# Performance work log

Measured on AMD Instinct MI355X. Metric: run time of the kernel, lower is better.

Reference implementation:

```python
import jax, jax.numpy as jnp
import numpy as np

N, E, G = 50000, 800000, 64   # nodes, edges, graphs
IN, HID, H = 128, 64, 4       # in_channels, hidden_channels, heads


def setup_inputs() -> dict:
    key = jax.random.key(0)
    ks = jax.random.split(key, 32)
    r = lambda i, shape, sc=0.05: jax.random.normal(ks[i], shape, jnp.float32) * sc
    inp = {
        "x": jax.random.normal(ks[0], (N, IN), jnp.float32),
        "edge_index": jax.random.randint(ks[1], (2, E), 0, N),
        "batch": jnp.sort(jax.random.randint(ks[2], (N,), 0, G)),
        # GATConv 1: in -> hidden, heads=4, concat
        "W1": r(3, (IN, H * HID)), "a_src1": r(4, (H, HID)), "a_dst1": r(5, (H, HID)), "b1": r(6, (H * HID,)),
        "bn1_g": 1.0 + r(7, (H * HID,)), "bn1_b": r(8, (H * HID,)), "bn1_m": r(9, (H * HID,)),
        "bn1_v": jax.random.uniform(ks[10], (H * HID,), jnp.float32, 0.5, 1.5),
        # GATConv 2: hidden*heads -> hidden, heads=4, concat
        "W2": r(11, (H * HID, H * HID)), "a_src2": r(12, (H, HID)), "a_dst2": r(13, (H, HID)), "b2": r(14, (H * HID,)),
        "bn2_g": 1.0 + r(15, (H * HID,)), "bn2_b": r(16, (H * HID,)), "bn2_m": r(17, (H * HID,)),
        "bn2_v": jax.random.uniform(ks[18], (H * HID,), jnp.float32, 0.5, 1.5),
        # GATConv 3: hidden*heads -> hidden, heads=1
        "W3": r(19, (H * HID, HID)), "a_src3": r(20, (1, HID)), "a_dst3": r(21, (1, HID)), "b3": r(22, (HID,)),
        # projection MLP: Linear(2*hidden, hidden) -> ReLU -> Linear(hidden, hidden)
        "P1": r(23, (2 * HID, HID)), "pb1": r(24, (HID,)),
        "P2": r(25, (HID, HID)), "pb2": r(26, (HID,)),
    }
    return inp


def _gat_conv(x, src, dst, n, W, a_s, a_d, b, concat):
    """PyG-style GATConv (eval mode). src/dst already include self-loops."""
    Hh, C = a_s.shape
    h = (x @ W).reshape(n, Hh, C)                       # [N, H, C]
    al_s = jnp.einsum('nhc,hc->nh', h, a_s)             # [N, H]
    al_d = jnp.einsum('nhc,hc->nh', h, a_d)             # [N, H]
    e = jax.nn.leaky_relu(al_s[src] + al_d[dst], 0.2)   # [E', H]
    # segment softmax over incoming edges of each dst node
    m = jax.ops.segment_max(e, dst, num_segments=n)     # [N, H] (finite: self-loops)
    ex = jnp.exp(e - m[dst])
    den = jax.ops.segment_sum(ex, dst, num_segments=n)
    alpha = ex / den[dst]                               # [E', H]
    out = jax.ops.segment_sum(h[src] * alpha[..., None], dst, num_segments=n)  # [N, H, C]
    out = out.reshape(n, Hh * C) if concat else out.mean(axis=1)
    return out + b


def _bn(x, g, b, m, v):
    return (x - m) * jax.lax.rsqrt(v + 1e-5) * g + b


def _forward(x, edge_index, batch,
             W1, a_src1, a_dst1, b1, bn1_g, bn1_b, bn1_m, bn1_v,
             W2, a_src2, a_dst2, b2, bn2_g, bn2_b, bn2_m, bn2_v,
             W3, a_src3, a_dst3, b3, P1, pb1, P2, pb2):
    n = x.shape[0]
    loop = jnp.arange(n)
    src = jnp.concatenate([edge_index[0], loop])        # add_self_loops=True
    dst = jnp.concatenate([edge_index[1], loop])
    h = _gat_conv(x, src, dst, n, W1, a_src1, a_dst1, b1, True)
    h = jax.nn.elu(_bn(h, bn1_g, bn1_b, bn1_m, bn1_v))  # dropout inactive in eval
    h = _gat_conv(h, src, dst, n, W2, a_src2, a_dst2, b2, True)
    h = jax.nn.elu(_bn(h, bn2_g, bn2_b, bn2_m, bn2_v))
    h = _gat_conv(h, src, dst, n, W3, a_src3, a_dst3, b3, False)  # heads=1
    x_max = jax.ops.segment_max(h, batch, num_segments=G)
    cnt = jax.ops.segment_sum(jnp.ones((n, 1), h.dtype), batch, num_segments=G)
    x_mean = jax.ops.segment_sum(h, batch, num_segments=G) / jnp.maximum(cnt, 1.0)
    z = jnp.concatenate([x_max, x_mean], axis=1)        # [G, 2*HID]
    z = jax.nn.relu(z @ P1 + pb1)
    return z @ P2 + pb2                                  # [G, HID]


def reference(x, edge_index, batch,
              W1, a_src1, a_dst1, b1, bn1_g, bn1_b, bn1_m, bn1_v,
              W2, a_src2, a_dst2, b2, bn2_g, bn2_b, bn2_m, bn2_v,
              W3, a_src3, a_dst3, b3, P1, pb1, P2, pb2):
    return _forward(x, edge_index, batch,
                    W1, a_src1, a_dst1, b1, bn1_g, bn1_b, bn1_m, bn1_v,
                    W2, a_src2, a_dst2, b2, bn2_g, bn2_b, bn2_m, bn2_v,
                    W3, a_src3, a_dst3, b3, P1, pb1, P2, pb2)
```

## Files before the change

### kernel.cpp

```cpp
#include <hip/hip_runtime.h>

typedef unsigned int uint;
typedef unsigned short ushort;

#define NFIX 50000
#define EFIX 800000
#define GFIX 64
#define BCAP 64
#define DCAP 128
#define WSTRIDE 136
#define PSL 16

__device__ __forceinline__ float bflo(uint u) { return __uint_as_float(u << 16); }
__device__ __forceinline__ float bfhi(uint u) { return __uint_as_float(u & 0xffff0000u); }
__device__ __forceinline__ float bf1(ushort u) { return __uint_as_float(((uint)u) << 16); }
__device__ __forceinline__ ushort f2bf(float f) {
    uint u = __float_as_uint(f);
    u += 0x7fffu + ((u >> 16) & 1u);
    return (ushort)(u >> 16);
}
__device__ __forceinline__ float lrelu(float x) { return fmaxf(x, 0.2f * x); }

typedef __attribute__((ext_vector_type(8))) short bf16x8;
typedef __attribute__((ext_vector_type(4))) float f32x4;
union U16B { uint4 u; bf16x8 v; };

__global__ void detect_idx_width(const int* __restrict__ ei, int* __restrict__ flag) {
    const int lane = threadIdx.x & 63;
    int v = (lane < 16) ? ei[2 * lane + 1] : 0;
    unsigned long long any = __ballot(v != 0);
    if (lane == 0 && blockIdx.x == 0) *flag = (any == 0ULL) ? 1 : 0;
}

__device__ __forceinline__ int ld_idx(const int* __restrict__ p, long i, int w64) {
    return w64 ? p[2 * i] : p[i];
}

__device__ __forceinline__ int frag_off(int k, int c, int K) {
    return ((c >> 4) * (K >> 5) + (k >> 5)) * 512 + ((c & 15) + 16 * ((k >> 3) & 3)) * 8 + (k & 7);
}

#define WJ1 (128 * 256)
#define WJ2 (256 * 256)
#define WJ3 (256 * 64)
#define BPJOBS (EFIX + WJ1 + WJ2 + WJ3)
__global__ void build_prep(const int* __restrict__ ei, const int* __restrict__ flag,
                           int* __restrict__ cnt, ushort* __restrict__ ssb,
                           const float* __restrict__ W1, ushort* __restrict__ Wf1,
                           const float* __restrict__ W2, ushort* __restrict__ Wf2,
                           const float* __restrict__ W3, ushort* __restrict__ Wf3) {
    int i = blockIdx.x * 256 + threadIdx.x;
    if (i < EFIX) {
        const int w64 = *flag;
        int d = ld_idx(ei, (long)EFIX + i, w64);
        int s = ld_idx(ei, i, w64);
        int slot = atomicAdd(&cnt[d], 1);
        if (slot < BCAP) ssb[d * BCAP + slot] = (ushort)s;
    } else {
        int j = i - EFIX;
        if (j < WJ1) {
            int k = j >> 8, c = j & 255;
            Wf1[frag_off(k, c, 128)] = f2bf(W1[j]);
        } else if ((j -= WJ1) < WJ2) {
            int k = j >> 8, c = j & 255;
            Wf2[frag_off(k, c, 256)] = f2bf(W2[j]);
        } else if ((j -= WJ2) < WJ3) {
            int k = j >> 6, c = j & 63;
            Wf3[frag_off(k, c, 256)] = f2bf(W3[j]);
        }
    }
}

template <int K, int NI, int HAL, bool F32A>
__global__ __launch_bounds__(256) void gemm_frag(const void* __restrict__ Xv,
                                                 const ushort* __restrict__ Wf,
                                                 const float* __restrict__ as_,
                                                 const float* __restrict__ ad_,
                                                 ushort* __restrict__ Hout,
                                                 float* __restrict__ als,
                                                 float* __restrict__ ald, int M) {
    constexpr int NC = NI * 16 * 4;
    constexpr int LOG2K = (K == 256) ? 8 : 7;
    __shared__ ushort sa[64][K + 8];
    __shared__ float s_ps[4][64];
    __shared__ float s_pd[4][64];

    const int tid = threadIdx.x;
    const int wave = tid >> 6;
    const int lane = tid & 63;
    const int rowBase = blockIdx.x * 64;
    const int colBase = wave * (NI * 16);
    const int tr = lane & 15;
    const int kq = (lane >> 4) * 8;

    if constexpr (F32A) {
        const float* srcf = (const float*)Xv;
#pragma unroll
        for (int it = 0; it < (64 * K) / 1024; ++it) {
            int linear = it * 1024 + tid * 4;
            int row = rowBase + (linear >> LOG2K);
            int col = linear & (K - 1);
            row = row < M ? row : M - 1;
            float4 v = *(const float4*)(srcf + (size_t)row * K + col);
            ushort4 o; o.x = f2bf(v.x); o.y = f2bf(v.y); o.z = f2bf(v.z); o.w = f2bf(v.w);
            *(ushort4*)(&sa[linear >> LOG2K][col]) = o;
        }
    } else {
        const ushort* src = (const ushort*)Xv + (size_t)rowBase * K;
#pragma unroll
        for (int it = 0; it < (64 * K) / 2048; ++it) {
            int linear = it * 2048 + tid * 8;
            int row = linear >> LOG2K;
            int col = linear & (K - 1);
            *(uint4*)(&sa[row][col]) = *(const uint4*)(src + linear);
        }
    }
    __syncthreads();

    f32x4 acc[4][NI];
#pragma unroll
    for (int i = 0; i < 4; ++i)
#pragma unroll
        for (int j = 0; j < NI; ++j) acc[i][j] = (f32x4){0.f, 0.f, 0.f, 0.f};

    const ushort* bp[NI];
#pragma unroll
    for (int ni = 0; ni < NI; ++ni)
        bp[ni] = Wf + ((size_t)(colBase / 16 + ni) * (K / 32)) * 512 + lane * 8;

    for (int k0 = 0; k0 < K; k0 += 32) {
        bf16x8 a[4], b[NI];
#pragma unroll
        for (int mi = 0; mi < 4; ++mi) { U16B t; t.u = *(const uint4*)(&sa[mi * 16 + tr][k0 + kq]); a[mi] = t.v; }
#pragma unroll
        for (int ni = 0; ni < NI; ++ni) { U16B t; t.u = *(const uint4*)(bp[ni] + (k0 >> 5) * 512); b[ni] = t.v; }
#pragma unroll
        for (int mi = 0; mi < 4; ++mi)
#pragma unroll
            for (int ni = 0; ni < NI; ++ni)
                acc[mi][ni] = __builtin_amdgcn_mfma_f32_16x16x32_bf16(a[mi], b[ni], acc[mi][ni], 0, 0, 0);
    }

    const int orow = (lane >> 4) * 4;
    const int ocol = colBase + tr;
#pragma unroll
    for (int mi = 0; mi < 4; ++mi) {
#pragma unroll
        for (int r = 0; r < 4; ++r) {
            int row = rowBase + mi * 16 + orow + r;
            if (row < M) {
#pragma unroll
                for (int ni = 0; ni < NI; ++ni)
                    Hout[(size_t)row * NC + ocol + ni * 16] = f2bf(acc[mi][ni][r]);
            }
        }
    }

    float asv[NI], adv[NI];
#pragma unroll
    for (int ni = 0; ni < NI; ++ni) {
        asv[ni] = as_[colBase + ni * 16 + tr];
        adv[ni] = ad_[colBase + ni * 16 + tr];
    }
#pragma unroll
    for (int mi = 0; mi < 4; ++mi) {
#pragma unroll
        for (int r = 0; r < 4; ++r) {
            float ps = 0.f, pd = 0.f;
#pragma unroll
            for (int ni = 0; ni < NI; ++ni) {
                ps += acc[mi][ni][r] * asv[ni];
                pd += acc[mi][ni][r] * adv[ni];
            }
#pragma unroll
            for (int off = 1; off < 16; off <<= 1) {
                ps += __shfl_xor(ps, off, 64);
                pd += __shfl_xor(pd, off, 64);
            }
            if constexpr (HAL == 4) {
                int row = rowBase + mi * 16 + orow + r;
                if (tr == 0 && row < M) {
                    als[(size_t)row * 4 + wave] = ps;
                    ald[(size_t)row * 4 + wave] = pd;
                }
            } else {
                if (tr == 0) {
                    s_ps[wave][mi * 16 + orow + r] = ps;
                    s_pd[wave][mi * 16 + orow + r] = pd;
                }
            }
        }
    }
    if constexpr (HAL == 1) {
        __syncthreads();
        if (tid < 64) {
            int row = rowBase + tid;
            if (row < M) {
                als[row] = s_ps[0][tid] + s_ps[1][tid] + s_ps[2][tid] + s_ps[3][tid];
                ald[row] = s_pd[0][tid] + s_pd[1][tid] + s_pd[2][tid] + s_pd[3][tid];
            }
        }
    }
}

template <int H_, int C>
__global__ __launch_bounds__(256) void gat_gather(
    const ushort* __restrict__ hb, const float* __restrict__ als, const float* __restrict__ ald,
    const int* __restrict__ cnt, const ushort* __restrict__ ssb,
    const float* __restrict__ bias, const float* __restrict__ bng, const float* __restrict__ bnb,
    const float* __restrict__ bnm, const float* __restrict__ bnv,
    ushort* __restrict__ xnext, int n) {
    constexpr int TC = H_ * C;
    constexpr int CPL = TC / 64;
    constexpr int GW = 64 / H_;
    constexpr int KMAX = DCAP / GW;
    constexpr int SHIFT = 8;
    __shared__ float s_w[4][H_ * WSTRIDE];
    __shared__ int s_idx[4][DCAP];
    const int wv = threadIdx.x >> 6;
    const int node = blockIdx.x * 4 + wv;
    if (node >= n) return;
    const int lane = threadIdx.x & 63;
    const int head = lane / GW;
    const int hl = lane & (GW - 1);
    const int c0 = lane * CPL;

    const float aldn = ald[(size_t)node * H_ + head];
    const float selfle = lrelu(als[(size_t)node * H_ + head] + aldn);
    const int e0 = node * BCAP;
    int d = cnt[node];
    d = d < BCAP ? d : BCAP;

    float acc[CPL];

    {
        float le_reg[KMAX];
        int s_reg[KMAX];
        float m = selfle;
#pragma unroll
        for (int k = 0; k < KMAX; ++k) {
            int j = hl + k * GW;
            if (j < d) {
                int s = ssb[e0 + j];
                s_reg[k] = s;
                float le = lrelu(als[(size_t)s * H_ + head] + aldn);
                le_reg[k] = le;
                m = fmaxf(m, le);
            }
        }
#pragma unroll
        for (int off = 1; off < GW; off <<= 1) m = fmaxf(m, __shfl_xor(m, off, 64));

        float dsum = (hl == 0) ? __expf(selfle - m) : 0.f;
#pragma unroll
        for (int k = 0; k < KMAX; ++k) {
            int j = hl + k * GW;
            if (j < d) {
                float p = __expf(le_reg[k] - m);
                dsum += p;
                s_w[wv][head * WSTRIDE + j] = p;
                if (head == 0) s_idx[wv][j] = s_reg[k] << SHIFT;
            }
        }
#pragma unroll
        for (int off = 1; off < GW; off <<= 1) dsum += __shfl_xor(dsum, off, 64);
        const float inv = 1.0f / dsum;

        {
            float psf = __expf(selfle - m);
            uint2 hu = *(const uint2*)(hb + (size_t)node * TC + c0);
            acc[0] = psf * bflo(hu.x); acc[1] = psf * bfhi(hu.x);
            acc[2] = psf * bflo(hu.y); acc[3] = psf * bfhi(hu.y);
        }
        const float* wbase = &s_w[wv][head * WSTRIDE];
        const int* ibase = &s_idx[wv][0];
        const ushort* hc = hb + c0;
        int j = 0;
        for (; j + 8 <= d; j += 8) {
            float4 wa = *(const float4*)(wbase + j);
            float4 wb2 = *(const float4*)(wbase + j + 4);
            int4 ia = *(const int4*)(ibase + j);
            int4 ib = *(const int4*)(ibase + j + 4);
            uint2 h0 = *(const uint2*)(hc + ia.x);
            uint2 h1 = *(const uint2*)(hc + ia.y);
            uint2 h2 = *(const uint2*)(hc + ia.z);
            uint2 h3 = *(const uint2*)(hc + ia.w);
            uint2 h4 = *(const uint2*)(hc + ib.x);
            uint2 h5 = *(const uint2*)(hc + ib.y);
            uint2 h6 = *(const uint2*)(hc + ib.z);
            uint2 h7 = *(const uint2*)(hc + ib.w);
            acc[0] = fmaf(wa.x, bflo(h0.x), acc[0]); acc[1] = fmaf(wa.x, bfhi(h0.x), acc[1]);
            acc[2] = fmaf(wa.x, bflo(h0.y), acc[2]); acc[3] = fmaf(wa.x, bfhi(h0.y), acc[3]);
            acc[0] = fmaf(wa.y, bflo(h1.x), acc[0]); acc[1] = fmaf(wa.y, bfhi(h1.x), acc[1]);
            acc[2] = fmaf(wa.y, bflo(h1.y), acc[2]); acc[3] = fmaf(wa.y, bfhi(h1.y), acc[3]);
            acc[0] = fmaf(wa.z, bflo(h2.x), acc[0]); acc[1] = fmaf(wa.z, bfhi(h2.x), acc[1]);
            acc[2] = fmaf(wa.z, bflo(h2.y), acc[2]); acc[3] = fmaf(wa.z, bfhi(h2.y), acc[3]);
            acc[0] = fmaf(wa.w, bflo(h3.x), acc[0]); acc[1] = fmaf(wa.w, bfhi(h3.x), acc[1]);
            acc[2] = fmaf(wa.w, bflo(h3.y), acc[2]); acc[3] = fmaf(wa.w, bfhi(h3.y), acc[3]);
            acc[0] = fmaf(wb2.x, bflo(h4.x), acc[0]); acc[1] = fmaf(wb2.x, bfhi(h4.x), acc[1]);
            acc[2] = fmaf(wb2.x, bflo(h4.y), acc[2]); acc[3] = fmaf(wb2.x, bfhi(h4.y), acc[3]);
            acc[0] = fmaf(wb2.y, bflo(h5.x), acc[0]); acc[1] = fmaf(wb2.y, bfhi(h5.x), acc[1]);
            acc[2] = fmaf(wb2.y, bflo(h5.y), acc[2]); acc[3] = fmaf(wb2.y, bfhi(h5.y), acc[3]);
            acc[0] = fmaf(wb2.z, bflo(h6.x), acc[0]); acc[1] = fmaf(wb2.z, bfhi(h6.x), acc[1]);
            acc[2] = fmaf(wb2.z, bflo(h6.y), acc[2]); acc[3] = fmaf(wb2.z, bfhi(h6.y), acc[3]);
            acc[0] = fmaf(wb2.w, bflo(h7.x), acc[0]); acc[1] = fmaf(wb2.w, bfhi(h7.x), acc[1]);
            acc[2] = fmaf(wb2.w, bflo(h7.y), acc[2]); acc[3] = fmaf(wb2.w, bfhi(h7.y), acc[3]);
        }
        for (; j + 4 <= d; j += 4) {
            float4 wa = *(const float4*)(wbase + j);
            int4 ia = *(const int4*)(ibase + j);
            uint2 h0 = *(const uint2*)(hc + ia.x);
            uint2 h1 = *(const uint2*)(hc + ia.y);
            uint2 h2 = *(const uint2*)(hc + ia.z);
            uint2 h3 = *(const uint2*)(hc + ia.w);
            acc[0] = fmaf(wa.x, bflo(h0.x), acc[0]); acc[1] = fmaf(wa.x, bfhi(h0.x), acc[1]);
            acc[2] = fmaf(wa.x, bflo(h0.y), acc[2]); acc[3] = fmaf(wa.x, bfhi(h0.y), acc[3]);
            acc[0] = fmaf(wa.y, bflo(h1.x), acc[0]); acc[1] = fmaf(wa.y, bfhi(h1.x), acc[1]);
            acc[2] = fmaf(wa.y, bflo(h1.y), acc[2]); acc[3] = fmaf(wa.y, bfhi(h1.y), acc[3]);
            acc[0] = fmaf(wa.z, bflo(h2.x), acc[0]); acc[1] = fmaf(wa.z, bfhi(h2.x), acc[1]);
            acc[2] = fmaf(wa.z, bflo(h2.y), acc[2]); acc[3] = fmaf(wa.z, bfhi(h2.y), acc[3]);
            acc[0] = fmaf(wa.w, bflo(h3.x), acc[0]); acc[1] = fmaf(wa.w, bfhi(h3.x), acc[1]);
            acc[2] = fmaf(wa.w, bflo(h3.y), acc[2]); acc[3] = fmaf(wa.w, bfhi(h3.y), acc[3]);
        }
        for (; j < d; ++j) {
            float w = wbase[j];
            int io = ibase[j];
            uint2 hu = *(const uint2*)(hc + io);
            acc[0] = fmaf(w, bflo(hu.x), acc[0]); acc[1] = fmaf(w, bfhi(hu.x), acc[1]);
            acc[2] = fmaf(w, bflo(hu.y), acc[2]); acc[3] = fmaf(w, bfhi(hu.y), acc[3]);
        }
#pragma unroll
        for (int q = 0; q < CPL; ++q) acc[q] *= inv;
    }

    float4 bi = *(const float4*)(bias + c0);
    float4 gg = *(const float4*)(bng + c0);
    float4 bb = *(const float4*)(bnb + c0);
    float4 mm = *(const float4*)(bnm + c0);
    float4 vv = *(const float4*)(bnv + c0);
    float biA[4] = { bi.x, bi.y, bi.z, bi.w };
    float ggA[4] = { gg.x, gg.y, gg.z, gg.w };
    float bbA[4] = { bb.x, bb.y, bb.z, bb.w };
    float mmA[4] = { mm.x, mm.y, mm.z, mm.w };
    float vvA[4] = { vv.x, vv.y, vv.z, vv.w };
    float r[4];
#pragma unroll
    for (int j2 = 0; j2 < 4; ++j2) {
        float v = acc[j2] + biA[j2];
        v = (v - mmA[j2]) * rsqrtf(vvA[j2] + 1e-5f) * ggA[j2] + bbA[j2];
        v = v > 0.f ? v : (__expf(v) - 1.0f);
        r[j2] = v;
    }
    uint p0 = (uint)f2bf(r[0]) | ((uint)f2bf(r[1]) << 16);
    uint p1 = (uint)f2bf(r[2]) | ((uint)f2bf(r[3]) << 16);
    uint2 o; o.x = p0; o.y = p1;
    *(uint2*)(xnext + (size_t)node * TC + c0) = o;
}

__global__ __launch_bounds__(256) void gat_gather_fin(
    const ushort* __restrict__ hb, const float* __restrict__ als, const float* __restrict__ ald,
    const int* __restrict__ cnt, const ushort* __restrict__ ssb,
    const float* __restrict__ bias, float* __restrict__ yout, int n) {
    __shared__ float s_w[4][BCAP + 16];
    __shared__ int s_idx[4][BCAP + 16];
    const int wv = threadIdx.x >> 6;
    const int node = blockIdx.x * 4 + wv;
    if (node >= n) return;
    const int lane = threadIdx.x & 63;
    const int es = lane >> 4;
    const int cq = (lane & 15) * 4;

    const float aldn = ald[node];
    const float selfle = lrelu(als[node] + aldn);
    const int e0 = node * BCAP;
    int d = cnt[node];
    d = d < BCAP ? d : BCAP;
    const int dpad = (d + 15) & ~15;

    float le = -3.0e38f;
    int sreg = 0;
    if (lane < d) {
        sreg = ssb[e0 + lane];
        le = lrelu(als[sreg] + aldn);
    }
    float m = fmaxf(le, selfle);
#pragma unroll
    for (int off = 1; off < 64; off <<= 1) m = fmaxf(m, __shfl_xor(m, off, 64));

    float p = 0.f;
    if (lane < d) {
        p = __expf(le - m);
        s_w[wv][lane] = p;
        s_idx[wv][lane] = sreg << 6;
    } else if (lane < dpad) {
        s_w[wv][lane] = 0.f;
        s_idx[wv][lane] = 0;
    }
    const float psf = __expf(selfle - m);
    float dsum = p + (lane == 0 ? psf : 0.f);
#pragma unroll
    for (int off = 1; off < 64; off <<= 1) dsum += __shfl_xor(dsum, off, 64);
    const float inv = 1.0f / dsum;

    const ushort* hp = hb + cq;
    const float* wbase = &s_w[wv][0];
    const int* ibase = &s_idx[wv][0];
    float a0 = 0.f, a1 = 0.f, a2 = 0.f, a3 = 0.f;
    for (int j = 0; j < d; j += 16) {
        int i0 = ibase[j + es];
        int i1 = ibase[j + 4 + es];
        int i2 = ibase[j + 8 + es];
        int i3 = ibase[j + 12 + es];
        uint2 h0 = *(const uint2*)(hp + i0);
        uint2 h1 = *(const uint2*)(hp + i1);
        uint2 h2 = *(const uint2*)(hp + i2);
        uint2 h3 = *(const uint2*)(hp + i3);
        float w0 = wbase[j + es];
        float w1 = wbase[j + 4 + es];
        float w2 = wbase[j + 8 + es];
        float w3 = wbase[j + 12 + es];
        a0 = fmaf(w0, bflo(h0.x), a0); a1 = fmaf(w0, bfhi(h0.x), a1);
        a2 = fmaf(w0, bflo(h0.y), a2); a3 = fmaf(w0, bfhi(h0.y), a3);
        a0 = fmaf(w1, bflo(h1.x), a0); a1 = fmaf(w1, bfhi(h1.x), a1);
        a2 = fmaf(w1, bflo(h1.y), a2); a3 = fmaf(w1, bfhi(h1.y), a3);
        a0 = fmaf(w2, bflo(h2.x), a0); a1 = fmaf(w2, bfhi(h2.x), a1);
        a2 = fmaf(w2, bflo(h2.y), a2); a3 = fmaf(w2, bfhi(h2.y), a3);
        a0 = fmaf(w3, bflo(h3.x), a0); a1 = fmaf(w3, bfhi(h3.x), a1);
        a2 = fmaf(w3, bflo(h3.y), a2); a3 = fmaf(w3, bfhi(h3.y), a3);
    }
#pragma unroll
    for (int off = 16; off < 64; off <<= 1) {
        a0 += __shfl_xor(a0, off, 64);
        a1 += __shfl_xor(a1, off, 64);
        a2 += __shfl_xor(a2, off, 64);
        a3 += __shfl_xor(a3, off, 64);
    }
    {
        uint2 hs = *(const uint2*)(hp + node * 64);
        a0 = (a0 + psf * bflo(hs.x)) * inv;
        a1 = (a1 + psf * bfhi(hs.x)) * inv;
        a2 = (a2 + psf * bflo(hs.y)) * inv;
        a3 = (a3 + psf * bfhi(hs.y)) * inv;
    }
    if (es == 0) {
        float4 o = { a0 + bias[cq + 0], a1 + bias[cq + 1],
                     a2 + bias[cq + 2], a3 + bias[cq + 3] };
        *(float4*)(yout + (size_t)node * 64 + cq) = o;
    }
}

__device__ __forceinline__ int lbound_w(const int* a, int n, int v, int w64) {
    int lo = 0, hi = n;
    while (lo < hi) {
        int mid = (lo + hi) >> 1;
        int bv = w64 ? a[2 * mid] : a[mid];
        if (bv < v) lo = mid + 1; else hi = mid;
    }
    return lo;
}

__global__ __launch_bounds__(256) void pool_part(const float* __restrict__ y, const int* __restrict__ batch,
                                                 const int* __restrict__ flag,
                                                 float* __restrict__ part) {
    const int w64 = *flag;
    const int g = blockIdx.x;
    const int sl = blockIdx.y;
    const int t = threadIdx.x;
    const int start = lbound_w(batch, NFIX, g, w64);
    const int end = lbound_w(batch, NFIX, g + 1, w64);
    const int len = end - start;
    const int s0 = start + (int)((long)len * sl / PSL);
    const int s1 = start + (int)((long)len * (sl + 1) / PSL);
    const int ch = t & 63, sub = t >> 6;
    float mx = -3.0e38f, sm = 0.f;
    for (int i = s0 + sub; i < s1; i += 4) {
        float v = y[(size_t)i * 64 + ch];
        mx = fmaxf(mx, v); sm += v;
    }
    __shared__ float smx[256], ssm[256];
    smx[t] = mx; ssm[t] = sm;
    __syncthreads();
    if (t < 64) {
        mx = fmaxf(fmaxf(smx[t], smx[t + 64]), fmaxf(smx[t + 128], smx[t + 192]));
        sm = ssm[t] + ssm[t + 64] + ssm[t + 128] + ssm[t + 192];
        float* pb = part + ((size_t)g * PSL + sl) * 128;
        pb[t] = mx;
        pb[64 + t] = sm;
    }
}

__global__ __launch_bounds__(64) void pool_fin_mlp(const float* __restrict__ part,
                                                   const int* __restrict__ batch,
                                                   const int* __restrict__ flag,
                                                   const float* __restrict__ P1, const float* __restrict__ pb1,
                                                   const float* __restrict__ P2, const float* __restrict__ pb2,
                                                   float* __restrict__ out) {
    const int w64 = *flag;
    const int g = blockIdx.x;
    const int t = threadIdx.x;
    const int start = lbound_w(batch, NFIX, g, w64);
    const int end = lbound_w(batch, NFIX, g + 1, w64);
    const int cnt = end - start;
    __shared__ float pl[128];
    __shared__ float z[64];
    float mx = -3.0e38f, sm = 0.f;
    const float* pb = part + (size_t)g * PSL * 128;
#pragma unroll
    for (int s = 0; s < PSL; ++s) {
        mx = fmaxf(mx, pb[s * 128 + t]);
        sm += pb[s * 128 + 64 + t];
    }
    float mean = cnt > 0 ? sm / (float)cnt : 0.f;
    if (cnt == 0) mx = 0.f;
    pl[t] = mx;
    pl[64 + t] = mean;
    __syncthreads();
    float a = pb1[t];
    for (int k = 0; k < 128; ++k) a = fmaf(pl[k], P1[k * 64 + t], a);
    z[t] = fmaxf(a, 0.f);
    __syncthreads();
    float o = pb2[t];
    for (int k = 0; k < 64; ++k) o = fmaf(z[k], P2[k * 64 + t], o);
    out[(size_t)g * 64 + t] = o;
}

__global__ void write_code(float* out, float code) {
    if (threadIdx.x == 0 && blockIdx.x == 0) out[0] = code;
}

extern "C" void kernel_launch(void* const* d_in, const int* in_sizes, int n_in,
                              void* d_out, int out_size, void* d_ws, size_t ws_size,
                              hipStream_t stream) {
    const float* x = (const float*)d_in[0];
    const int* ei = (const int*)d_in[1];
    const int* batch = (const int*)d_in[2];
    const float* W1 = (const float*)d_in[3];
    const float* as1 = (const float*)d_in[4];
    const float* ad1 = (const float*)d_in[5];
    const float* b1 = (const float*)d_in[6];
    const float* bn1g = (const float*)d_in[7];
    const float* bn1b = (const float*)d_in[8];
    const float* bn1m = (const float*)d_in[9];
    const float* bn1v = (const float*)d_in[10];
    const float* W2 = (const float*)d_in[11];
    const float* as2 = (const float*)d_in[12];
    const float* ad2 = (const float*)d_in[13];
    const float* b2 = (const float*)d_in[14];
    const float* bn2g = (const float*)d_in[15];
    const float* bn2b = (const float*)d_in[16];
    const float* bn2m = (const float*)d_in[17];
    const float* bn2v = (const float*)d_in[18];
    const float* W3 = (const float*)d_in[19];
    const float* as3 = (const float*)d_in[20];
    const float* ad3 = (const float*)d_in[21];
    const float* b3 = (const float*)d_in[22];
    const float* P1 = (const float*)d_in[23];
    const float* pb1 = (const float*)d_in[24];
    const float* P2 = (const float*)d_in[25];
    const float* pb2 = (const float*)d_in[26];
    float* out = (float*)d_out;
    (void)n_in; (void)out_size; (void)in_sizes;

    const int N_ = NFIX;

    char* ws = (char*)d_ws;
    size_t off = 0;
    auto alloc = [&](size_t bytes) -> void* {
        void* p = ws + off;
        off = (off + bytes + 255) & ~(size_t)255;
        return p;
    };
    ushort* hbuf = (ushort*)alloc((size_t)N_ * 256 * 2);
    ushort* xbuf = (ushort*)alloc((size_t)N_ * 256 * 2);
    float* als = (float*)alloc((size_t)N_ * 4 * 4);
    float* ald = (float*)alloc((size_t)N_ * 4 * 4);
    int* cnt = (int*)alloc((size_t)N_ * 4);
    ushort* ssb = (ushort*)alloc((size_t)N_ * BCAP * 2);
    ushort* Wf1 = (ushort*)alloc(128 * 256 * 2);
    ushort* Wf2 = (ushort*)alloc(256 * 256 * 2);
    ushort* Wf3 = (ushort*)alloc(256 * 64 * 2);
    float* part = (float*)alloc((size_t)GFIX * PSL * 128 * 4);
    int* flag = (int*)alloc(256);
    float* y3 = (float*)xbuf;
    const size_t needed = off;

    if (ws_size < needed) {
        write_code<<<1, 64, 0, stream>>>(out, 1000.0f + (float)(needed >> 20));
        return;
    }

    const int ng4 = (N_ + 3) / 4;
    const int rb64 = (N_ + 63) / 64;
    const int bpg = (BPJOBS + 255) / 256;

    detect_idx_width<<<1, 64, 0, stream>>>(ei, flag);
    hipMemsetAsync(cnt, 0, (size_t)N_ * 4, stream);
    build_prep<<<bpg, 256, 0, stream>>>(ei, flag, cnt, ssb, W1, Wf1, W2, Wf2, W3, Wf3);

    gemm_frag<128, 4, 4, true><<<rb64, 256, 0, stream>>>(x, Wf1, as1, ad1, hbuf, als, ald, N_);
    gat_gather<4, 64><<<ng4, 256, 0, stream>>>(hbuf, als, ald, cnt, ssb,
                                               b1, bn1g, bn1b, bn1m, bn1v, xbuf, N_);
    gemm_frag<256, 4, 4, false><<<rb64, 256, 0, stream>>>(xbuf, Wf2, as2, ad2, hbuf, als, ald, N_);
    gat_gather<4, 64><<<ng4, 256, 0, stream>>>(hbuf, als, ald, cnt, ssb,
                                               b2, bn2g, bn2b, bn2m, bn2v, xbuf, N_);
    gemm_frag<256, 1, 1, false><<<rb64, 256, 0, stream>>>(xbuf, Wf3, as3, ad3, hbuf, als, ald, N_);
    gat_gather_fin<<<ng4, 256, 0, stream>>>(hbuf, als, ald, cnt, ssb, b3, y3, N_);

    pool_part<<<dim3(GFIX, PSL), 256, 0, stream>>>(y3, batch, flag, part);
    pool_fin_mlp<<<GFIX, 64, 0, stream>>>(part, batch, flag, P1, pb1, P2, pb2, out);
}
```

Before: 394.6 us.

## Fuse edge bucketing and W2/W3 conversion into first GEMM launch

```diff
diff --git a/kernel.cpp b/kernel.cpp
--- a/kernel.cpp
+++ b/kernel.cpp
@@ -25,13 +25,6 @@
 typedef __attribute__((ext_vector_type(4))) float f32x4;
 union U16B { uint4 u; bf16x8 v; };
 
-__global__ void detect_idx_width(const int* __restrict__ ei, int* __restrict__ flag) {
-    const int lane = threadIdx.x & 63;
-    int v = (lane < 16) ? ei[2 * lane + 1] : 0;
-    unsigned long long any = __ballot(v != 0);
-    if (lane == 0 && blockIdx.x == 0) *flag = (any == 0ULL) ? 1 : 0;
-}
-
 __device__ __forceinline__ int ld_idx(const int* __restrict__ p, long i, int w64) {
     return w64 ? p[2 * i] : p[i];
 }
@@ -43,36 +36,150 @@
 #define WJ1 (128 * 256)
 #define WJ2 (256 * 256)
 #define WJ3 (256 * 64)
-#define BPJOBS (EFIX + WJ1 + WJ2 + WJ3)
-__global__ void build_prep(const int* __restrict__ ei, const int* __restrict__ flag,
-                           int* __restrict__ cnt, ushort* __restrict__ ssb,
-                           const float* __restrict__ W1, ushort* __restrict__ Wf1,
-                           const float* __restrict__ W2, ushort* __restrict__ Wf2,
-                           const float* __restrict__ W3, ushort* __restrict__ Wf3) {
-    int i = blockIdx.x * 256 + threadIdx.x;
-    if (i < EFIX) {
-        const int w64 = *flag;
-        int d = ld_idx(ei, (long)EFIX + i, w64);
-        int s = ld_idx(ei, i, w64);
-        int slot = atomicAdd(&cnt[d], 1);
-        if (slot < BCAP) ssb[d * BCAP + slot] = (ushort)s;
-    } else {
-        int j = i - EFIX;
-        if (j < WJ1) {
-            int k = j >> 8, c = j & 255;
-            Wf1[frag_off(k, c, 128)] = f2bf(W1[j]);
-        } else if ((j -= WJ1) < WJ2) {
-            int k = j >> 8, c = j & 255;
-            Wf2[frag_off(k, c, 256)] = f2bf(W2[j]);
-        } else if ((j -= WJ2) < WJ3) {
-            int k = j >> 6, c = j & 63;
-            Wf3[frag_off(k, c, 256)] = f2bf(W3[j]);
-        }
-    }
-}
-
-template <int K, int NI, int HAL, bool F32A>
-__global__ __launch_bounds__(256) void gemm_frag(const void* __restrict__ Xv,
+#define SCJOBS (EFIX + WJ2 + WJ3)
+
+__global__ void pre_w1_detect(const int* __restrict__ ei, int* __restrict__ flag,
+                              const float* __restrict__ W1, ushort* __restrict__ Wf1) {
+    if (blockIdx.x == gridDim.x - 1) {
+        const int lane = threadIdx.x & 63;
+        if (threadIdx.x < 64) {
+            int v = (lane < 16) ? ei[2 * lane + 1] : 0;
+            unsigned long long any = __ballot(v != 0);
+            if (lane == 0) *flag = (any == 0ULL) ? 1 : 0;
+        }
+        return;
+    }
+    int j = blockIdx.x * 256 + threadIdx.x;
+    int k = j >> 8, c = j & 255;
+    Wf1[frag_off(k, c, 128)] = f2bf(W1[j]);
+}
+
+__global__ __launch_bounds__(256) void gemm1_build(
+    const float* __restrict__ x, const ushort* __restrict__ Wf,
+    const float* __restrict__ as_, const float* __restrict__ ad_,
+    ushort* __restrict__ Hout, float* __restrict__ als, float* __restrict__ ald,
+    int M, int gemmBlocks,
+    const int* __restrict__ ei, const int* __restrict__ flag,
+    int* __restrict__ cnt, ushort* __restrict__ ssb,
+    const float* __restrict__ W2, ushort* __restrict__ Wf2,
+    const float* __restrict__ W3, ushort* __restrict__ Wf3) {
+    constexpr int K = 128;
+    constexpr int NI = 4;
+    constexpr int LOG2K = 7;
+    __shared__ ushort sa[64][K + 8];
+
+    if (blockIdx.x >= gemmBlocks) {
+        int i = (blockIdx.x - gemmBlocks) * 256 + threadIdx.x;
+        if (i < EFIX) {
+            const int w64 = *flag;
+            int d = ld_idx(ei, (long)EFIX + i, w64);
+            int s = ld_idx(ei, i, w64);
+            int slot = atomicAdd(&cnt[d], 1);
+            if (slot < BCAP) ssb[d * BCAP + slot] = (ushort)s;
+        } else {
+            int j = i - EFIX;
+            if (j < WJ2) {
+                int k = j >> 8, c = j & 255;
+                Wf2[frag_off(k, c, 256)] = f2bf(W2[j]);
+            } else if ((j -= WJ2) < WJ3) {
+                int k = j >> 6, c = j & 63;
+                Wf3[frag_off(k, c, 256)] = f2bf(W3[j]);
+            }
+        }
+        return;
+    }
+
+    const int tid = threadIdx.x;
+    const int wave = tid >> 6;
+    const int lane = tid & 63;
+    const int rowBase = blockIdx.x * 64;
+    const int colBase = wave * (NI * 16);
+    const int tr = lane & 15;
+    const int kq = (lane >> 4) * 8;
+
+#pragma unroll
+    for (int it = 0; it < (64 * K) / 1024; ++it) {
+        int linear = it * 1024 + tid * 4;
+        int row = rowBase + (linear >> LOG2K);
+        int col = linear & (K - 1);
+        row = row < M ? row : M - 1;
+        float4 v = *(const float4*)(x + (size_t)row * K + col);
+        ushort4 o; o.x = f2bf(v.x); o.y = f2bf(v.y); o.z = f2bf(v.z); o.w = f2bf(v.w);
+        *(ushort4*)(&sa[linear >> LOG2K][col]) = o;
+    }
+    __syncthreads();
+
+    f32x4 acc[4][NI];
+#pragma unroll
+    for (int i = 0; i < 4; ++i)
+#pragma unroll
+        for (int j = 0; j < NI; ++j) acc[i][j] = (f32x4){0.f, 0.f, 0.f, 0.f};
+
+    const ushort* bp[NI];
+#pragma unroll
+    for (int ni = 0; ni < NI; ++ni)
+        bp[ni] = Wf + ((size_t)(colBase / 16 + ni) * (K / 32)) * 512 + lane * 8;
+
+    for (int k0 = 0; k0 < K; k0 += 32) {
+        bf16x8 a[4], b[NI];
+#pragma unroll
+        for (int mi = 0; mi < 4; ++mi) { U16B t; t.u = *(const uint4*)(&sa[mi * 16 + tr][k0 + kq]); a[mi] = t.v; }
+#pragma unroll
+        for (int ni = 0; ni < NI; ++ni) { U16B t; t.u = *(const uint4*)(bp[ni] + (k0 >> 5) * 512); b[ni] = t.v; }
+#pragma unroll
+        for (int mi = 0; mi < 4; ++mi)
+#pragma unroll
+            for (int ni = 0; ni < NI; ++ni)
+                acc[mi][ni] = __builtin_amdgcn_mfma_f32_16x16x32_bf16(a[mi], b[ni], acc[mi][ni], 0, 0, 0);
+    }
+
+    const int orow = (lane >> 4) * 4;
+    const int ocol = colBase + tr;
+#pragma unroll
+    for (int mi = 0; mi < 4; ++mi) {
+#pragma unroll
+        for (int r = 0; r < 4; ++r) {
+            int row = rowBase + mi * 16 + orow + r;
+            if (row < M) {
+#pragma unroll
+                for (int ni = 0; ni < NI; ++ni)
+                    Hout[(size_t)row * 256 + ocol + ni * 16] = f2bf(acc[mi][ni][r]);
+            }
+        }
+    }
+
+    float asv[NI], adv[NI];
+#pragma unroll
+    for (int ni = 0; ni < NI; ++ni) {
+        asv[ni] = as_[colBase + ni * 16 + tr];
+        adv[ni] = ad_[colBase + ni * 16 + tr];
+    }
+#pragma unroll
+    for (int mi = 0; mi < 4; ++mi) {
+#pragma unroll
+        for (int r = 0; r < 4; ++r) {
+            float ps = 0.f, pd = 0.f;
+#pragma unroll
+            for (int ni = 0; ni < NI; ++ni) {
+                ps += acc[mi][ni][r] * asv[ni];
+                pd += acc[mi][ni][r] * adv[ni];
+            }
+#pragma unroll
+            for (int off = 1; off < 16; off <<= 1) {
+                ps += __shfl_xor(ps, off, 64);
+                pd += __shfl_xor(pd, off, 64);
+            }
+            int row = rowBase + mi * 16 + orow + r;
+            if (tr == 0 && row < M) {
+                als[(size_t)row * 4 + wave] = ps;
+                ald[(size_t)row * 4 + wave] = pd;
+            }
+        }
+    }
+}
+
+template <int K, int NI, int HAL>
+__global__ __launch_bounds__(256) void gemm_frag(const ushort* __restrict__ X,
                                                  const ushort* __restrict__ Wf,
                                                  const float* __restrict__ as_,
                                                  const float* __restrict__ ad_,
@@ -93,27 +200,13 @@
     const int tr = lane & 15;
     const int kq = (lane >> 4) * 8;
 
-    if constexpr (F32A) {
-        const float* srcf = (const float*)Xv;
-#pragma unroll
-        for (int it = 0; it < (64 * K) / 1024; ++it) {
-            int linear = it * 1024 + tid * 4;
-            int row = rowBase + (linear >> LOG2K);
-            int col = linear & (K - 1);
-            row = row < M ? row : M - 1;
-            float4 v = *(const float4*)(srcf + (size_t)row * K + col);
-            ushort4 o; o.x = f2bf(v.x); o.y = f2bf(v.y); o.z = f2bf(v.z); o.w = f2bf(v.w);
-            *(ushort4*)(&sa[linear >> LOG2K][col]) = o;
-        }
-    } else {
-        const ushort* src = (const ushort*)Xv + (size_t)rowBase * K;
-#pragma unroll
-        for (int it = 0; it < (64 * K) / 2048; ++it) {
-            int linear = it * 2048 + tid * 8;
-            int row = linear >> LOG2K;
-            int col = linear & (K - 1);
-            *(uint4*)(&sa[row][col]) = *(const uint4*)(src + linear);
-        }
+    const ushort* src = X + (size_t)rowBase * K;
+#pragma unroll
+    for (int it = 0; it < (64 * K) / 2048; ++it) {
+        int linear = it * 2048 + tid * 8;
+        int row = linear >> LOG2K;
+        int col = linear & (K - 1);
+        *(uint4*)(&sa[row][col]) = *(const uint4*)(src + linear);
     }
     __syncthreads();
 
@@ -591,19 +684,21 @@
 
     const int ng4 = (N_ + 3) / 4;
     const int rb64 = (N_ + 63) / 64;
-    const int bpg = (BPJOBS + 255) / 256;
-
-    detect_idx_width<<<1, 64, 0, stream>>>(ei, flag);
+    const int scg = (SCJOBS + 255) / 256;
+    const int wg1 = WJ1 / 256 + 1;
+
     hipMemsetAsync(cnt, 0, (size_t)N_ * 4, stream);
-    build_prep<<<bpg, 256, 0, stream>>>(ei, flag, cnt, ssb, W1, Wf1, W2, Wf2, W3, Wf3);
-
-    gemm_frag<128, 4, 4, true><<<rb64, 256, 0, stream>>>(x, Wf1, as1, ad1, hbuf, als, ald, N_);
+    pre_w1_detect<<<wg1, 256, 0, stream>>>(ei, flag, W1, Wf1);
+
+    gemm1_build<<<rb64 + scg, 256, 0, stream>>>(x, Wf1, as1, ad1, hbuf, als, ald,
+                                                N_, rb64, ei, flag, cnt, ssb,
+                                                W2, Wf2, W3, Wf3);
     gat_gather<4, 64><<<ng4, 256, 0, stream>>>(hbuf, als, ald, cnt, ssb,
                                                b1, bn1g, bn1b, bn1m, bn1v, xbuf, N_);
-    gemm_frag<256, 4, 4, false><<<rb64, 256, 0, stream>>>(xbuf, Wf2, as2, ad2, hbuf, als, ald, N_);
+    gemm_frag<256, 4, 4><<<rb64, 256, 0, stream>>>(xbuf, Wf2, as2, ad2, hbuf, als, ald, N_);
     gat_gather<4, 64><<<ng4, 256, 0, stream>>>(hbuf, als, ald, cnt, ssb,
                                                b2, bn2g, bn2b, bn2m, bn2v, xbuf, N_);
-    gemm_frag<256, 1, 1, false><<<rb64, 256, 0, stream>>>(xbuf, Wf3, as3, ad3, hbuf, als, ald, N_);
+    gemm_frag<256, 1, 1><<<rb64, 256, 0, stream>>>(xbuf, Wf3, as3, ad3, hbuf, als, ald, N_);
     gat_gather_fin<<<ng4, 256, 0, stream>>>(hbuf, als, ald, cnt, ssb, b3, y3, N_);
 
     pool_part<<<dim3(GFIX, PSL), 256, 0, stream>>>(y3, batch, flag, part);
```

Result: faster. 383.0 us, median of 2 (-3.0%).
